# Performance work log

Measured on AMD Instinct MI355X. Metric: run time of the kernel, lower is better.

## Reference

```python
import jax, jax.numpy as jnp
import numpy as np

TEMPERATURE = 0.07
BASE_TEMPERATURE = 0.07
NUM_HEADS = 4


def setup_inputs() -> dict:
    key = jax.random.key(0)
    k1, k2 = jax.random.split(key)
    features = jax.random.normal(k1, (2048, 2, 256), dtype=jnp.float32)
    labels = jax.random.randint(k2, (2048, 10), 0, 2).astype(jnp.float32)
    return {"features": features, "labels": labels}


def reference(features, labels):
    B, V, E = features.shape
    H = NUM_HEADS
    fs = E // H
    N = B * V

    # torch.cat(torch.unbind(features, dim=1), dim=0): view-major stacking
    f = jnp.transpose(features, (1, 0, 2)).reshape(N, H, fs)
    # F.normalize(dim=-1) with eps=1e-12 clamp
    norm = jnp.sqrt(jnp.sum(f * f, axis=-1, keepdims=True))
    f = f / jnp.maximum(norm, 1e-12)

    # per-head pairwise similarities: dot[i, j, h] = <f[i,h], f[j,h]>  (N, N, H)
    dot = jnp.einsum('ihf,jhf->ijh', f, f)
    heads = jnp.argmax(dot, axis=-1)              # (N, N) head chosen per (anchor, positive)
    dotT = dot / TEMPERATURE

    # logits_max is over j for fixed (i, head); detached in the original
    maxh = jax.lax.stop_gradient(jnp.max(dotT, axis=1))   # (N, H)

    # positive mask, tiled across views, self removed
    mask = (labels @ labels.T) > 0                # (B, B) bool
    mask = jnp.tile(mask, (V, V)).astype(f.dtype)  # (N, N)
    logits_mask = 1.0 - jnp.eye(N, dtype=f.dtype)  # (N, N)
    mask = mask * logits_mask

    # masked exp-sum per (anchor, head): S[i,h] = sum_j lm[i,j] * exp(dotT[i,j,h] - maxh[i,h])
    exp_l = jnp.exp(dotT - maxh[:, None, :])       # (N, N, H)
    S = jnp.einsum('ij,ijh->ih', logits_mask, exp_l)  # (N, H)
    logS = jnp.log(S)

    # select per-pair head: log_prob[i,k] = dotT[i,k,h(i,k)] - maxh[i,h(i,k)] - logS[i,h(i,k)]
    dot_sel = jnp.take_along_axis(dotT, heads[..., None], axis=2)[..., 0]  # (N, N)
    max_sel = jnp.take_along_axis(maxh, heads, axis=1)                     # (N, N)
    logS_sel = jnp.take_along_axis(logS, heads, axis=1)                    # (N, N)
    log_prob = dot_sel - max_sel - logS_sel

    mean_log_prob_pos = jnp.sum(mask * log_prob, axis=1) / jnp.sum(mask, axis=1)
    loss = -(TEMPERATURE / BASE_TEMPERATURE) * mean_log_prob_pos

    finite = jnp.isfinite(loss)
    return jnp.sum(jnp.where(finite, loss, 0.0)) / jnp.sum(finite)
```

## Files before the change

### kernel.cpp

```cpp
#include <hip/hip_runtime.h>
#include <math.h>

#define BS    2048
#define NROW  4096
#define EDIM  256
#define INVT  (1.0f/0.07f)

typedef float  float4v __attribute__((ext_vector_type(4)));
typedef short  short8v __attribute__((ext_vector_type(8)));

static __device__ __forceinline__ unsigned short f2bf(float x) {
    unsigned u = __builtin_bit_cast(unsigned, x);
    u += 0x7fffu + ((u >> 16) & 1u);
    return (unsigned short)(u >> 16);
}

static __device__ __forceinline__ void gload_lds16(const void* g, void* l) {
    __builtin_amdgcn_global_load_lds(
        (const __attribute__((address_space(1))) unsigned int*)g,
        (__attribute__((address_space(3))) unsigned int*)l, 16, 0, 0);
}

__global__ void prep_kernel(const float* __restrict__ feat, const float* __restrict__ labels,
                            unsigned short* __restrict__ fnb, unsigned* __restrict__ bits,
                            float* __restrict__ zacc) {
    const int b = blockIdx.x, t = threadIdx.x;
    if (b < NROW) {
        int bb = b & (BS - 1);
        int v = b >> 11;
        float x = feat[(size_t)bb * (2 * EDIM) + (size_t)v * EDIM + t];
        float ss = x * x;
#pragma unroll
        for (int off = 32; off > 0; off >>= 1)
            ss += __shfl_xor(ss, off, 64);
        float nrm = fmaxf(sqrtf(ss), 1e-12f);
        fnb[(size_t)b * EDIM + t] = f2bf(x / nrm);
    } else {
        int g = (b - NROW) * 256 + t;
        unsigned bb = 0;
#pragma unroll
        for (int d = 0; d < 10; ++d)
            bb |= (labels[g * 10 + d] != 0.0f ? 1u : 0u) << d;
        bits[g] = bb;
        for (int k = g; k < NROW * 9 + 3; k += 2048) zacc[k] = 0.0f;
    }
}

__global__ __launch_bounds__(256, 3) void main_kernel(
    const unsigned short* __restrict__ fnb, const unsigned* __restrict__ bits,
    float* __restrict__ S, float* __restrict__ Num, float* __restrict__ Cnt) {

    __shared__ unsigned short shB[64 * 256];

    const int tid  = threadIdx.x;
    const int lane = tid & 63;
    const int wave = tid >> 6;
    const int quad = lane >> 4;
    const int ml   = lane & 15;
    const int xr   = ml & 7;
    const int i0   = blockIdx.x * 64 + wave * 16;
    const int jc0  = blockIdx.y * 256;

    short8v af[4][2];
    {
        const unsigned short* ap = fnb + (size_t)(i0 + ml) * EDIM + quad * 8;
#pragma unroll
        for (int h = 0; h < 4; ++h)
#pragma unroll
            for (int kk = 0; kk < 2; ++kk)
                af[h][kk] = *(const short8v*)(ap + h * 64 + kk * 32);
    }

    unsigned ibr[4];
#pragma unroll
    for (int r = 0; r < 4; ++r)
        ibr[r] = bits[(i0 + quad * 4 + r) & (BS - 1)];

    float    Sp[4][4] = {};
    float    np[4] = {};
    unsigned cpk[4] = {};

    for (int t = 0; t < 4; ++t) {
        const int j0 = jc0 + t * 64;
        __syncthreads();
#pragma unroll
        for (int q = 0; q < 8; ++q) {
            const int G   = tid + 256 * q;
            const int row = G >> 5;
            const int gg  = (G & 31) ^ (row & 7);
            gload_lds16(fnb + (size_t)(j0 + row) * EDIM + gg * 8, shB + G * 8);
        }
        __syncthreads();

        unsigned jbr[4];
#pragma unroll
        for (int js = 0; js < 4; ++js)
            jbr[js] = bits[(j0 + js * 16 + ml) & (BS - 1)];

        float4v dacc[4][4];
#pragma unroll
        for (int js = 0; js < 4; ++js)
#pragma unroll
            for (int h = 0; h < 4; ++h)
                dacc[js][h] = (float4v){0.f, 0.f, 0.f, 0.f};

#pragma unroll
        for (int h = 0; h < 4; ++h)
#pragma unroll
            for (int kk = 0; kk < 2; ++kk) {
                const int gsw = ((h * 8 + kk * 4 + quad) ^ xr) * 8;
#pragma unroll
                for (int js = 0; js < 4; ++js) {
                    short8v bf = *(const short8v*)(shB + (js * 16 + ml) * 256 + gsw);
                    dacc[js][h] = __builtin_amdgcn_mfma_f32_16x16x32_bf16(af[h][kk], bf, dacc[js][h], 0, 0, 0);
                }
            }

#pragma unroll
        for (int r = 0; r < 4; ++r) {
            const int i = i0 + quad * 4 + r;
            const unsigned ibit = ibr[r];
#pragma unroll
            for (int js = 0; js < 4; ++js) {
                const int j = j0 + js * 16 + ml;
                const float d0 = dacc[js][0][r];
                const float d1 = dacc[js][1][r];
                const float d2 = dacc[js][2][r];
                const float d3 = dacc[js][3][r];
                float bd = d0; int bh = 0;
                if (d1 > bd) { bd = d1; bh = 1; }
                if (d2 > bd) { bd = d2; bh = 2; }
                if (d3 > bd) { bd = d3; bh = 3; }
                const bool off = (i != j);
                const float e0 = __expf(fmaf(d0, INVT, -INVT));
                const float e1 = __expf(fmaf(d1, INVT, -INVT));
                const float e2 = __expf(fmaf(d2, INVT, -INVT));
                const float e3 = __expf(fmaf(d3, INVT, -INVT));
                if (off) {
                    Sp[r][0] += e0; Sp[r][1] += e1; Sp[r][2] += e2; Sp[r][3] += e3;
                }
                if (off && (ibit & jbr[js])) {
                    np[r] += bd;
                    cpk[r] += 1u << (bh * 8);
                }
            }
        }
    }

#pragma unroll
    for (int r = 0; r < 4; ++r) {
        const int i = i0 + quad * 4 + r;
        float v[9];
        v[0] = np[r];
#pragma unroll
        for (int h = 0; h < 4; ++h) v[1 + h] = Sp[r][h];
#pragma unroll
        for (int h = 0; h < 4; ++h) v[5 + h] = (float)((cpk[r] >> (8 * h)) & 255u);
#pragma unroll
        for (int k = 0; k < 9; ++k) {
            float x = v[k];
            x += __shfl_xor(x, 1, 64);
            x += __shfl_xor(x, 2, 64);
            x += __shfl_xor(x, 4, 64);
            x += __shfl_xor(x, 8, 64);
            v[k] = x;
        }
        if (ml == 0) {
            atomicAdd(&Num[i], v[0] * INVT);
#pragma unroll
            for (int h = 0; h < 4; ++h) atomicAdd(&S[i * 4 + h], v[1 + h]);
#pragma unroll
            for (int h = 0; h < 4; ++h) atomicAdd(&Cnt[i * 4 + h], v[5 + h]);
        }
    }
}

__global__ void final_kernel(const float* __restrict__ S, const float* __restrict__ Num,
                             const float* __restrict__ Cnt, float* __restrict__ red,
                             unsigned* __restrict__ done, float* __restrict__ out) {
    const int tid = threadIdx.x;
    const int i = blockIdx.x * 256 + tid;
    float c = 0.f;
    float numr = Num[i];
#pragma unroll
    for (int h = 0; h < 4; ++h) {
        float sh = S[i * 4 + h];
        float ch = Cnt[i * 4 + h];
        numr -= ch * (INVT + logf(sh));
        c += ch;
    }
    float ls = 0.f, lc = 0.f;
    if (c > 0.f) { ls = -(numr / c); lc = 1.f; }

    __shared__ float rs[256], rc[256];
    rs[tid] = ls; rc[tid] = lc;
    __syncthreads();
    for (int s = 128; s > 0; s >>= 1) {
        if (tid < s) { rs[tid] += rs[tid + s]; rc[tid] += rc[tid + s]; }
        __syncthreads();
    }
    if (tid == 0) {
        atomicAdd(&red[0], rs[0]);
        atomicAdd(&red[1], rc[0]);
        __threadfence();
        if (atomicAdd(done, 1u) == 15u) {
            float s = atomicAdd(&red[0], 0.0f);
            float cc = atomicAdd(&red[1], 0.0f);
            out[0] = s / cc;
        }
    }
}

extern "C" void kernel_launch(void* const* d_in, const int* in_sizes, int n_in,
                              void* d_out, int out_size, void* d_ws, size_t ws_size,
                              hipStream_t stream) {
    const float* feat = (const float*)d_in[0];
    const float* labels = (const float*)d_in[1];
    float* out = (float*)d_out;

    char* ws = (char*)d_ws;
    unsigned short* fnb = (unsigned short*)ws;
    float* S = (float*)(ws + (size_t)NROW * EDIM * sizeof(unsigned short));
    float* Num = S + NROW * 4;
    float* Cnt = Num + NROW;
    float* red = Cnt + NROW * 4;
    unsigned* done = (unsigned*)(red + 2);
    unsigned* bits = done + 1;

    prep_kernel<<<NROW + 8, 256, 0, stream>>>(feat, labels, fnb, bits, S);
    main_kernel<<<dim3(64, 16), 256, 0, stream>>>(fnb, bits, S, Num, Cnt);
    final_kernel<<<16, 256, 0, stream>>>(S, Num, Cnt, red, done, out);
}
```

Measured before the change: 116.4 us.

## Double-buffer B tiles in LDS and fuse final reduction into main kernel

The main kernel now streams 32-row B tiles through two LDS buffers, so the load for the next tile is issued while MFMAs run on the current one. Occupancy is raised to 4 blocks per CU. The separate final kernel is removed: the last block to finish, found with an atomic counter, computes the loss and the global mean. This saves one launch and hides load latency, at the cost of smaller per-tile MFMA batches and a serial tail done by a single block.

After: 170.5 us. +46.6%, slower.

```diff
diff --git a/kernel.cpp b/kernel.cpp
--- a/kernel.cpp
+++ b/kernel.cpp
@@ -5,6 +5,7 @@
 #define NROW  4096
 #define EDIM  256
 #define INVT  (1.0f/0.07f)
+#define NBLK  (64*16)
 
 typedef float  float4v __attribute__((ext_vector_type(4)));
 typedef short  short8v __attribute__((ext_vector_type(8)));
@@ -46,11 +47,14 @@
     }
 }
 
-__global__ __launch_bounds__(256, 3) void main_kernel(
+__global__ __launch_bounds__(256, 4) void main_kernel(
     const unsigned short* __restrict__ fnb, const unsigned* __restrict__ bits,
-    float* __restrict__ S, float* __restrict__ Num, float* __restrict__ Cnt) {
-
-    __shared__ unsigned short shB[64 * 256];
+    float* __restrict__ S, float* __restrict__ Num, float* __restrict__ Cnt,
+    unsigned* __restrict__ done, float* __restrict__ out) {
+
+    __shared__ unsigned short shB[2][32 * 256];
+    __shared__ float rwave[8];
+    __shared__ unsigned lastFlag;
 
     const int tid  = threadIdx.x;
     const int lane = tid & 63;
@@ -80,26 +84,33 @@
     float    np[4] = {};
     unsigned cpk[4] = {};
 
-    for (int t = 0; t < 4; ++t) {
-        const int j0 = jc0 + t * 64;
-        __syncthreads();
-#pragma unroll
-        for (int q = 0; q < 8; ++q) {
+    auto STAGE = [&](int st, int buf) {
+#pragma unroll
+        for (int q = 0; q < 4; ++q) {
             const int G   = tid + 256 * q;
             const int row = G >> 5;
             const int gg  = (G & 31) ^ (row & 7);
-            gload_lds16(fnb + (size_t)(j0 + row) * EDIM + gg * 8, shB + G * 8);
-        }
-        __syncthreads();
-
-        unsigned jbr[4];
-#pragma unroll
-        for (int js = 0; js < 4; ++js)
+            gload_lds16(fnb + (size_t)(jc0 + st * 32 + row) * EDIM + gg * 8,
+                        &shB[buf][G * 8]);
+        }
+    };
+
+    STAGE(0, 0);
+    __syncthreads();
+
+    for (int st = 0; st < 8; ++st) {
+        const int cur = st & 1;
+        if (st < 7) STAGE(st + 1, cur ^ 1);
+
+        const int j0 = jc0 + st * 32;
+        unsigned jbr[2];
+#pragma unroll
+        for (int js = 0; js < 2; ++js)
             jbr[js] = bits[(j0 + js * 16 + ml) & (BS - 1)];
 
-        float4v dacc[4][4];
-#pragma unroll
-        for (int js = 0; js < 4; ++js)
+        float4v dacc[2][4];
+#pragma unroll
+        for (int js = 0; js < 2; ++js)
 #pragma unroll
             for (int h = 0; h < 4; ++h)
                 dacc[js][h] = (float4v){0.f, 0.f, 0.f, 0.f};
@@ -110,8 +121,8 @@
             for (int kk = 0; kk < 2; ++kk) {
                 const int gsw = ((h * 8 + kk * 4 + quad) ^ xr) * 8;
 #pragma unroll
-                for (int js = 0; js < 4; ++js) {
-                    short8v bf = *(const short8v*)(shB + (js * 16 + ml) * 256 + gsw);
+                for (int js = 0; js < 2; ++js) {
+                    short8v bf = *(const short8v*)(&shB[cur][(js * 16 + ml) * 256 + gsw]);
                     dacc[js][h] = __builtin_amdgcn_mfma_f32_16x16x32_bf16(af[h][kk], bf, dacc[js][h], 0, 0, 0);
                 }
             }
@@ -121,7 +132,7 @@
             const int i = i0 + quad * 4 + r;
             const unsigned ibit = ibr[r];
 #pragma unroll
-            for (int js = 0; js < 4; ++js) {
+            for (int js = 0; js < 2; ++js) {
                 const int j = j0 + js * 16 + ml;
                 const float d0 = dacc[js][0][r];
                 const float d1 = dacc[js][1][r];
@@ -145,6 +156,7 @@
                 }
             }
         }
+        __syncthreads();
     }
 
 #pragma unroll
@@ -173,41 +185,35 @@
             for (int h = 0; h < 4; ++h) atomicAdd(&Cnt[i * 4 + h], v[5 + h]);
         }
     }
-}
-
-__global__ void final_kernel(const float* __restrict__ S, const float* __restrict__ Num,
-                             const float* __restrict__ Cnt, float* __restrict__ red,
-                             unsigned* __restrict__ done, float* __restrict__ out) {
-    const int tid = threadIdx.x;
-    const int i = blockIdx.x * 256 + tid;
-    float c = 0.f;
-    float numr = Num[i];
-#pragma unroll
-    for (int h = 0; h < 4; ++h) {
-        float sh = S[i * 4 + h];
-        float ch = Cnt[i * 4 + h];
-        numr -= ch * (INVT + logf(sh));
-        c += ch;
-    }
-    float ls = 0.f, lc = 0.f;
-    if (c > 0.f) { ls = -(numr / c); lc = 1.f; }
-
-    __shared__ float rs[256], rc[256];
-    rs[tid] = ls; rc[tid] = lc;
+
+    __threadfence();
     __syncthreads();
-    for (int s = 128; s > 0; s >>= 1) {
-        if (tid < s) { rs[tid] += rs[tid + s]; rc[tid] += rc[tid + s]; }
+    if (tid == 0) lastFlag = (atomicAdd(done, 1u) == NBLK - 1) ? 1u : 0u;
+    __syncthreads();
+    if (lastFlag) {
+        float ls = 0.f, lc = 0.f;
+        for (int r2 = tid; r2 < NROW; r2 += 256) {
+            float numr = __hip_atomic_load(&Num[r2], __ATOMIC_RELAXED, __HIP_MEMORY_SCOPE_AGENT);
+            float c = 0.f;
+#pragma unroll
+            for (int h = 0; h < 4; ++h) {
+                float sh = __hip_atomic_load(&S[r2 * 4 + h], __ATOMIC_RELAXED, __HIP_MEMORY_SCOPE_AGENT);
+                float ch = __hip_atomic_load(&Cnt[r2 * 4 + h], __ATOMIC_RELAXED, __HIP_MEMORY_SCOPE_AGENT);
+                numr -= ch * (INVT + logf(sh));
+                c += ch;
+            }
+            if (c > 0.f) { ls -= numr / c; lc += 1.f; }
+        }
+#pragma unroll
+        for (int off2 = 32; off2 > 0; off2 >>= 1) {
+            ls += __shfl_xor(ls, off2, 64);
+            lc += __shfl_xor(lc, off2, 64);
+        }
+        if (lane == 0) { rwave[wave] = ls; rwave[4 + wave] = lc; }
         __syncthreads();
-    }
-    if (tid == 0) {
-        atomicAdd(&red[0], rs[0]);
-        atomicAdd(&red[1], rc[0]);
-        __threadfence();
-        if (atomicAdd(done, 1u) == 15u) {
-            float s = atomicAdd(&red[0], 0.0f);
-            float cc = atomicAdd(&red[1], 0.0f);
-            out[0] = s / cc;
-        }
+        if (tid == 0)
+            out[0] = (rwave[0] + rwave[1] + rwave[2] + rwave[3]) /
+                     (rwave[4] + rwave[5] + rwave[6] + rwave[7]);
     }
 }
 
@@ -228,6 +234,5 @@
     unsigned* bits = done + 1;
 
     prep_kernel<<<NROW + 8, 256, 0, stream>>>(feat, labels, fnb, bits, S);
-    main_kernel<<<dim3(64, 16), 256, 0, stream>>>(fnb, bits, S, Num, Cnt);
-    final_kernel<<<16, 256, 0, stream>>>(S, Num, Cnt, red, done, out);
-}
+    main_kernel<<<dim3(64, 16), 256, 0, stream>>>(fnb, bits, S, Num, Cnt, done, out);
+}
```

## Double-buffer LDS B tiles in 32-row stages and raise occupancy target

Applied to the files above, without the earlier changes.

Splits each 256-column chunk into eight 32-row stages held in two LDS buffers, issuing the async global-to-LDS load for the next stage before computing on the current one, so memory latency overlaps MFMA and epilogue work. Accumulators shrink from 4x4 to 4 float4 per inner step, which cuts register pressure and allows raising launch bounds to 4 blocks per CU. The trade-off is one barrier per stage instead of two per 64-row tile, and smaller MFMA batches per barrier. The wait for the prefetched load relies on the end-of-iteration __syncthreads draining the outstanding LDS DMA.

After: 109.4 us. -6.0%, faster.

```diff
diff --git a/kernel.cpp b/kernel.cpp
--- a/kernel.cpp
+++ b/kernel.cpp
@@ -46,11 +46,11 @@
     }
 }
 
-__global__ __launch_bounds__(256, 3) void main_kernel(
+__global__ __launch_bounds__(256, 4) void main_kernel(
     const unsigned short* __restrict__ fnb, const unsigned* __restrict__ bits,
     float* __restrict__ S, float* __restrict__ Num, float* __restrict__ Cnt) {
 
-    __shared__ unsigned short shB[64 * 256];
+    __shared__ unsigned short shB[2][32 * 256];
 
     const int tid  = threadIdx.x;
     const int lane = tid & 63;
@@ -80,53 +80,49 @@
     float    np[4] = {};
     unsigned cpk[4] = {};
 
-    for (int t = 0; t < 4; ++t) {
-        const int j0 = jc0 + t * 64;
-        __syncthreads();
-#pragma unroll
-        for (int q = 0; q < 8; ++q) {
+    auto STAGE = [&](int st, int buf) {
+#pragma unroll
+        for (int q = 0; q < 4; ++q) {
             const int G   = tid + 256 * q;
             const int row = G >> 5;
             const int gg  = (G & 31) ^ (row & 7);
-            gload_lds16(fnb + (size_t)(j0 + row) * EDIM + gg * 8, shB + G * 8);
-        }
-        __syncthreads();
-
-        unsigned jbr[4];
-#pragma unroll
-        for (int js = 0; js < 4; ++js)
-            jbr[js] = bits[(j0 + js * 16 + ml) & (BS - 1)];
-
-        float4v dacc[4][4];
-#pragma unroll
-        for (int js = 0; js < 4; ++js)
+            gload_lds16(fnb + (size_t)(jc0 + st * 32 + row) * EDIM + gg * 8,
+                        &shB[buf][G * 8]);
+        }
+    };
+
+    STAGE(0, 0);
+    __syncthreads();
+
+    for (int st = 0; st < 8; ++st) {
+        const int cur = st & 1;
+        if (st < 7) STAGE(st + 1, cur ^ 1);
+        const int j0 = jc0 + st * 32;
+
+#pragma unroll
+        for (int js = 0; js < 2; ++js) {
+            const unsigned jb = bits[(j0 + js * 16 + ml) & (BS - 1)];
+
+            float4v dacc[4];
+#pragma unroll
+            for (int h = 0; h < 4; ++h) dacc[h] = (float4v){0.f, 0.f, 0.f, 0.f};
 #pragma unroll
             for (int h = 0; h < 4; ++h)
-                dacc[js][h] = (float4v){0.f, 0.f, 0.f, 0.f};
-
-#pragma unroll
-        for (int h = 0; h < 4; ++h)
-#pragma unroll
-            for (int kk = 0; kk < 2; ++kk) {
-                const int gsw = ((h * 8 + kk * 4 + quad) ^ xr) * 8;
-#pragma unroll
-                for (int js = 0; js < 4; ++js) {
-                    short8v bf = *(const short8v*)(shB + (js * 16 + ml) * 256 + gsw);
-                    dacc[js][h] = __builtin_amdgcn_mfma_f32_16x16x32_bf16(af[h][kk], bf, dacc[js][h], 0, 0, 0);
+#pragma unroll
+                for (int kk = 0; kk < 2; ++kk) {
+                    const int gsw = ((h * 8 + kk * 4 + quad) ^ xr) * 8;
+                    short8v bf = *(const short8v*)(&shB[cur][(js * 16 + ml) * 256 + gsw]);
+                    dacc[h] = __builtin_amdgcn_mfma_f32_16x16x32_bf16(af[h][kk], bf, dacc[h], 0, 0, 0);
                 }
-            }
-
-#pragma unroll
-        for (int r = 0; r < 4; ++r) {
-            const int i = i0 + quad * 4 + r;
-            const unsigned ibit = ibr[r];
-#pragma unroll
-            for (int js = 0; js < 4; ++js) {
-                const int j = j0 + js * 16 + ml;
-                const float d0 = dacc[js][0][r];
-                const float d1 = dacc[js][1][r];
-                const float d2 = dacc[js][2][r];
-                const float d3 = dacc[js][3][r];
+
+            const int j = j0 + js * 16 + ml;
+#pragma unroll
+            for (int r = 0; r < 4; ++r) {
+                const int i = i0 + quad * 4 + r;
+                const float d0 = dacc[0][r];
+                const float d1 = dacc[1][r];
+                const float d2 = dacc[2][r];
+                const float d3 = dacc[3][r];
                 float bd = d0; int bh = 0;
                 if (d1 > bd) { bd = d1; bh = 1; }
                 if (d2 > bd) { bd = d2; bh = 2; }
@@ -139,12 +135,13 @@
                 if (off) {
                     Sp[r][0] += e0; Sp[r][1] += e1; Sp[r][2] += e2; Sp[r][3] += e3;
                 }
-                if (off && (ibit & jbr[js])) {
+                if (off && (ibr[r] & jb)) {
                     np[r] += bd;
                     cpk[r] += 1u << (bh * 8);
                 }
             }
         }
+        __syncthreads();
     }
 
 #pragma unroll
```
